# Performance work log

Hardware: AMD Instinct MI355X
Metric: run time of the kernel (lower is better)

Reference implementation:

```python
import jax, jax.numpy as jnp
import numpy as np

B, N, EM = 16, 1024, 768
D_K, D_V, H = 768, 768, 12

def setup_inputs() -> dict:
    key = jax.random.key(0)
    ks = jax.random.split(key, 4)
    s = 0.02
    x = jax.random.normal(ks[0], (B, N, EM), dtype=jnp.float32)
    W_qk = jax.random.normal(ks[1], (EM, 2 * D_K), dtype=jnp.float32) * s
    b_qk = jnp.zeros((2 * D_K,), dtype=jnp.float32)
    W_v = jax.random.normal(ks[2], (EM, D_V), dtype=jnp.float32) * s
    b_v = jnp.zeros((D_V,), dtype=jnp.float32)
    W_proj = jax.random.normal(ks[3], (D_V, EM), dtype=jnp.float32) * s
    b_proj = jnp.zeros((EM,), dtype=jnp.float32)
    return {"x": x, "W_qk": W_qk, "b_qk": b_qk, "W_v": W_v, "b_v": b_v,
            "W_proj": W_proj, "b_proj": b_proj}

def reference(x, W_qk, b_qk, W_v, b_v, W_proj, b_proj):
    b, n, _ = x.shape
    d = D_K // H  # per-head dim
    # qk Linear -> [B,N,2*d_K]; rearrange 'b n (h d qk) -> qk b h n d'
    # i.e. last dim splits as (h, d, 2) with qk fastest-varying.
    qk = (x @ W_qk + b_qk).reshape(b, n, H, d, 2)
    Q = jnp.transpose(qk[..., 0], (0, 2, 1, 3))  # [B,H,N,d]
    K = jnp.transpose(qk[..., 1], (0, 2, 1, 3))  # [B,H,N,d]
    V = (x @ W_v + b_v).reshape(b, n, H, D_V // H).transpose(0, 2, 1, 3)  # [B,H,N,dv]
    scores = jnp.einsum('bhqd,bhkd->bhqk', Q, K) / jnp.sqrt(jnp.float32(d))
    att = jax.nn.softmax(scores, axis=-1)  # dropout p=0 -> identity
    out = jnp.einsum('bhqk,bhkv->bhqv', att, V)  # [B,H,N,dv]
    out = out.transpose(0, 2, 1, 3).reshape(b, n, D_V)
    return out @ W_proj + b_proj
```

## Files before the change

kernel.cpp:

```cpp
#include <hip/hip_runtime.h>
#include <hip/hip_bf16.h>
#include <stdint.h>

typedef unsigned short u16;
typedef __bf16 bf16_t;
typedef bf16_t bf16x8 __attribute__((ext_vector_type(8)));
typedef short s16x4 __attribute__((ext_vector_type(4)));
typedef float f32x4 __attribute__((ext_vector_type(4)));

__device__ __forceinline__ float bf2f(u16 u) {
    union { uint32_t i; float f; } v; v.i = ((uint32_t)u) << 16; return v.f;
}
__device__ __forceinline__ u16 f2bf(float f) {
    union { float f; uint32_t i; } v; v.f = f;
    uint32_t i = v.i;
    uint32_t r = (i + 0x7FFFu + ((i >> 16) & 1u)) >> 16;
    return (u16)r;
}

__device__ __forceinline__ void gload_lds16(const u16* g, u16* l) {
    auto gp = (const __attribute__((address_space(1))) void*)g;
    auto lp = (__attribute__((address_space(3))) void*)(uintptr_t)l;
    __builtin_amdgcn_global_load_lds(gp, lp, 16, 0, 0);
}

__global__ void convert_f32_bf16_kernel(const float* __restrict__ src,
                                        u16* __restrict__ dst, int n4) {
    int i = blockIdx.x * blockDim.x + threadIdx.x;
    if (i < n4) {
        float4 v = ((const float4*)src)[i];
        ushort4 o;
        o.x = f2bf(v.x); o.y = f2bf(v.y); o.z = f2bf(v.z); o.w = f2bf(v.w);
        ((ushort4*)dst)[i] = o;
    }
}

__global__ void transpose_qk_kernel(const float* __restrict__ W, const float* __restrict__ b,
                                    u16* __restrict__ Wt, float* __restrict__ bp) {
    int r = blockIdx.x;
    int qk = (r >= 768) ? 1 : 0;
    int hd = r - qk * 768;
    int c = (hd >> 6) * 128 + (hd & 63) * 2 + qk;
    float s = qk ? 1.0f : 0.125f;
    for (int k = threadIdx.x; k < 768; k += 256)
        Wt[r * 768 + k] = f2bf(s * W[k * 1536 + c]);
    if (threadIdx.x == 0) bp[r] = s * b[c];
}

__global__ void transpose_sq_kernel(const float* __restrict__ W, u16* __restrict__ Wt) {
    int n = blockIdx.x;
    for (int k = threadIdx.x; k < 768; k += 256)
        Wt[n * 768 + k] = f2bf(W[k * 768 + n]);
}

#define BM 128
#define BN 128
#define BK 32
#define LDT 40

template<int MODE>
__global__ __launch_bounds__(256)
void gemm_bt_kernel(const u16* __restrict__ A, const u16* __restrict__ Bt,
                    const float* __restrict__ bias, void* __restrict__ Cout,
                    void* __restrict__ Cout2, int M, int N, int K) {
    __shared__ __attribute__((aligned(16))) u16 As[BM * LDT];
    __shared__ __attribute__((aligned(16))) u16 Bs[BN * LDT];

    const int tid  = threadIdx.x;
    const int lane = tid & 63;
    const int wave = tid >> 6;
    const int l16  = lane & 15;
    const int quad = lane >> 4;
    const int m0 = blockIdx.y * BM;
    const int n0 = blockIdx.x * BN;
    const int wm = (wave & 1) * 64;
    const int wn = (wave >> 1) * 64;

    f32x4 acc[4][4];
#pragma unroll
    for (int i = 0; i < 4; i++)
#pragma unroll
        for (int j = 0; j < 4; j++) acc[i][j] = (f32x4){0.f, 0.f, 0.f, 0.f};

    const int r0  = tid >> 2;
    const int seg = tid & 3;

    for (int k0 = 0; k0 < K; k0 += BK) {
        const u16* Ag = A  + (size_t)(m0 + r0) * K + k0 + seg * 8;
        const u16* Bg = Bt + (size_t)(n0 + r0) * K + k0 + seg * 8;
        int4 a0 = *(const int4*)Ag;
        int4 a1 = *(const int4*)(Ag + (size_t)64 * K);
        int4 b0 = *(const int4*)Bg;
        int4 b1 = *(const int4*)(Bg + (size_t)64 * K);
        *(int4*)&As[r0 * LDT + seg * 8]        = a0;
        *(int4*)&As[(r0 + 64) * LDT + seg * 8] = a1;
        *(int4*)&Bs[r0 * LDT + seg * 8]        = b0;
        *(int4*)&Bs[(r0 + 64) * LDT + seg * 8] = b1;
        __syncthreads();

        bf16x8 af[4], bfr[4];
#pragma unroll
        for (int i = 0; i < 4; i++) {
            af[i]  = *(const bf16x8*)&As[(wm + i * 16 + l16) * LDT + quad * 8];
            bfr[i] = *(const bf16x8*)&Bs[(wn + i * 16 + l16) * LDT + quad * 8];
        }
#pragma unroll
        for (int i = 0; i < 4; i++)
#pragma unroll
            for (int j = 0; j < 4; j++)
                acc[i][j] = __builtin_amdgcn_mfma_f32_16x16x32_bf16(af[i], bfr[j], acc[i][j], 0, 0, 0);
        __syncthreads();
    }

#pragma unroll
    for (int j = 0; j < 4; j++) {
        int cnb = n0 + wn + j * 16;
        int cn  = cnb + l16;
        float bv = bias[cn];
#pragma unroll
        for (int i = 0; i < 4; i++) {
            int cm = m0 + wm + i * 16 + quad * 4;
            if constexpr (MODE == 3) {
                int h  = cnb >> 6;
                int dv = (cnb & 63) + l16;
                int b  = cm >> 10, n = cm & 1023;
                ushort4 o;
                o.x = f2bf(acc[i][j][0] + bv);
                o.y = f2bf(acc[i][j][1] + bv);
                o.z = f2bf(acc[i][j][2] + bv);
                o.w = f2bf(acc[i][j][3] + bv);
                *(ushort4*)&((u16*)Cout)[((size_t)((b * 12 + h) * 64 + dv)) * 1024 + n] = o;
            } else if constexpr (MODE == 2) {
                int qk = cnb >= 768;
                int hd = cnb - qk * 768;
                int h  = hd >> 6;
                int d  = (hd & 63) + l16;
                int b  = cm >> 10, n = cm & 1023;
                u16* dst = (u16*)(qk ? Cout2 : Cout);
#pragma unroll
                for (int r = 0; r < 4; r++)
                    dst[((size_t)((b * 12 + h) * 1024 + n + r)) * 64 + d] =
                        f2bf(acc[i][j][r] + bv);
            } else {
#pragma unroll
                for (int r = 0; r < 4; r++) {
                    float val = acc[i][j][r] + bv;
                    if constexpr (MODE == 1)
                        ((float*)Cout)[(size_t)(cm + r) * N + cn] = val;
                    else
                        ((u16*)Cout)[(size_t)(cm + r) * N + cn] = f2bf(val);
                }
            }
        }
    }
}

__global__ __launch_bounds__(256)
void attention_mfma_kernel(const u16* __restrict__ Qp, const u16* __restrict__ Kp,
                           const u16* __restrict__ Vp, u16* __restrict__ attout) {
    __shared__ __attribute__((aligned(16))) u16 Ks[64 * 64];
    __shared__ __attribute__((aligned(16))) u16 Vs[64 * 64];

    const int tid  = threadIdx.x;
    const int wave = tid >> 6;
    const int lane = tid & 63;
    const int l16  = lane & 15;
    const int quad = lane >> 4;
    const int bh = blockIdx.y;
    const int b  = bh / 12, h = bh % 12;
    const int head = b * 12 + h;
    const int q0 = blockIdx.x * 128 + wave * 32;

    const u16* Qhead = Qp + (size_t)head * 1024 * 64;
    const u16* Khead = Kp + (size_t)head * 1024 * 64;
    const u16* Vhead = Vp + (size_t)head * 64 * 1024;

    bf16x8 qf[2][2];
#pragma unroll
    for (int qb = 0; qb < 2; qb++) {
        const u16* qrow = Qhead + (size_t)(q0 + qb * 16 + l16) * 64;
        qf[qb][0] = *(const bf16x8*)(qrow + quad * 8);
        qf[qb][1] = *(const bf16x8*)(qrow + 32 + quad * 8);
    }

    f32x4 oacc[2][4];
#pragma unroll
    for (int qb = 0; qb < 2; qb++)
#pragma unroll
        for (int db = 0; db < 4; db++) oacc[qb][db] = (f32x4){0.f, 0.f, 0.f, 0.f};
    float l_part[2] = {0.f, 0.f};

    const int srow = tid >> 3;
    const int gseg = (tid & 7) ^ (srow & 7);
    u16* KsW = Ks + wave * 512;
    u16* VsW = Vs + wave * 512;
    const int sw7 = l16 & 7;

    for (int kt = 0; kt < 1024; kt += 64) {
        gload_lds16(Khead + (size_t)(kt + srow) * 64 + gseg * 8,        KsW);
        gload_lds16(Khead + (size_t)(kt + 32 + srow) * 64 + gseg * 8,   KsW + 2048);
        gload_lds16(Vhead + (size_t)srow * 1024 + kt + gseg * 8,        VsW);
        gload_lds16(Vhead + (size_t)(32 + srow) * 1024 + kt + gseg * 8, VsW + 2048);
        __syncthreads();

        s16x4 pf[2][4];
        {
            bf16x8 kf[4][2];
#pragma unroll
            for (int jb = 0; jb < 4; jb++) {
#pragma unroll
                for (int hf = 0; hf < 2; hf++)
                    kf[jb][hf] = *(const bf16x8*)&Ks[(jb * 16 + l16) * 64 +
                                                     (((hf * 4 + quad) ^ sw7) * 8)];
            }
#pragma unroll
            for (int qb = 0; qb < 2; qb++) {
#pragma unroll
                for (int jb = 0; jb < 4; jb++) {
                    f32x4 st = (f32x4){0.f, 0.f, 0.f, 0.f};
                    st = __builtin_amdgcn_mfma_f32_16x16x32_bf16(kf[jb][0], qf[qb][0], st, 0, 0, 0);
                    st = __builtin_amdgcn_mfma_f32_16x16x32_bf16(kf[jb][1], qf[qb][1], st, 0, 0, 0);
                    float e0 = __expf(st[0]), e1 = __expf(st[1]);
                    float e2 = __expf(st[2]), e3 = __expf(st[3]);
                    l_part[qb] += (e0 + e1) + (e2 + e3);
                    union { __hip_bfloat162 h2; uint32_t u; } c0, c1;
                    c0.h2 = __float22bfloat162_rn(make_float2(e0, e1));
                    c1.h2 = __float22bfloat162_rn(make_float2(e2, e3));
                    union { uint32_t u2[2]; s16x4 v; } pk;
                    pk.u2[0] = c0.u; pk.u2[1] = c1.u;
                    pf[qb][jb] = pk.v;
                }
            }
        }

#pragma unroll
        for (int db = 0; db < 4; db++) {
            s16x4 vb[4];
#pragma unroll
            for (int jb = 0; jb < 4; jb++) {
                int g = jb * 2 + (quad >> 1);
                vb[jb] = *(const s16x4*)&Vs[(db * 16 + l16) * 64 +
                                            ((g ^ sw7) * 8) + (quad & 1) * 4];
            }
#pragma unroll
            for (int qb = 0; qb < 2; qb++)
#pragma unroll
                for (int jb = 0; jb < 4; jb++)
                    oacc[qb][db] = __builtin_amdgcn_mfma_f32_16x16x16bf16_1k(
                        pf[qb][jb], vb[jb], oacc[qb][db], 0, 0, 0);
        }
        __syncthreads();
    }

#pragma unroll
    for (int qb = 0; qb < 2; qb++) {
        float l = l_part[qb];
        l += __shfl_xor(l, 16);
        l += __shfl_xor(l, 32);
        float linv[4];
#pragma unroll
        for (int r = 0; r < 4; r++)
            linv[r] = 1.0f / __shfl(l, quad * 4 + r);
        u16* orow = attout + (size_t)(b * 1024 + q0 + qb * 16 + quad * 4) * 768 + h * 64 + l16;
#pragma unroll
        for (int db = 0; db < 4; db++)
#pragma unroll
            for (int r = 0; r < 4; r++)
                orow[(size_t)r * 768 + db * 16] = f2bf(oacc[qb][db][r] * linv[r]);
    }
}

extern "C" void kernel_launch(void* const* d_in, const int* in_sizes, int n_in,
                              void* d_out, int out_size, void* d_ws, size_t ws_size,
                              hipStream_t stream) {
    const float* x      = (const float*)d_in[0];
    const float* W_qk   = (const float*)d_in[1];
    const float* b_qk   = (const float*)d_in[2];
    const float* W_v    = (const float*)d_in[3];
    const float* b_v    = (const float*)d_in[4];
    const float* W_proj = (const float*)d_in[5];
    const float* b_proj = (const float*)d_in[6];
    float* out = (float*)d_out;

    char* ws = (char*)d_ws;
    size_t off = 0;
    auto alloc = [&](size_t bytes) { void* p = ws + off; off += (bytes + 255) & ~255ull; return p; };
    u16*   xb     = (u16*)alloc((size_t)16384 * 768 * 2);
    u16*   Wqkt   = (u16*)alloc((size_t)1536 * 768 * 2);
    float* bqkp   = (float*)alloc(1536 * 4);
    u16*   Wvt    = (u16*)alloc((size_t)768 * 768 * 2);
    u16*   Wprojt = (u16*)alloc((size_t)768 * 768 * 2);
    u16*   Qp     = (u16*)alloc((size_t)16384 * 768 * 2);
    u16*   Kp     = (u16*)alloc((size_t)16384 * 768 * 2);
    u16*   Vp     = (u16*)alloc((size_t)16384 * 768 * 2);
    u16*   attout = (u16*)alloc((size_t)16384 * 768 * 2);

    convert_f32_bf16_kernel<<<12288, 256, 0, stream>>>(x, xb, 3145728);
    transpose_qk_kernel<<<1536, 256, 0, stream>>>(W_qk, b_qk, Wqkt, bqkp);
    transpose_sq_kernel<<<768, 256, 0, stream>>>(W_v, Wvt);
    transpose_sq_kernel<<<768, 256, 0, stream>>>(W_proj, Wprojt);

    gemm_bt_kernel<2><<<dim3(12, 128), 256, 0, stream>>>(xb, Wqkt, bqkp, Qp, Kp, 16384, 1536, 768);
    gemm_bt_kernel<3><<<dim3(6, 128), 256, 0, stream>>>(xb, Wvt, b_v, Vp, nullptr, 16384, 768, 768);
    attention_mfma_kernel<<<dim3(8, 192), 256, 0, stream>>>(Qp, Kp, Vp, attout);
    gemm_bt_kernel<1><<<dim3(6, 128), 256, 0, stream>>>(attout, Wprojt, b_proj, out, nullptr, 16384, 768, 768);
}
```

Measured before the change: 364.7 us.

## Use direct global-to-LDS loads in GEMM, vectorize epilogues, widen attention blocks

The GEMM kernel now stages A and B tiles with global_load_lds instead of register round-trips, using an XOR-swizzled unpadded LDS layout to avoid bank conflicts. For non-V modes it swaps the MFMA operands so each lane holds four consecutive output columns, which allows float4 bias loads and ushort4/float4 vectorized stores. Attention blocks grow to 512 threads covering 256 queries, so each K/V tile loaded into LDS is shared by twice as many waves and each thread issues half as many loads. Risks include lower occupancy from the larger blocks and the unchanged single-buffered GEMM loop still stalling on each barrier.

```diff
diff --git a/kernel.cpp b/kernel.cpp
--- a/kernel.cpp
+++ b/kernel.cpp
@@ -8,9 +8,6 @@
 typedef short s16x4 __attribute__((ext_vector_type(4)));
 typedef float f32x4 __attribute__((ext_vector_type(4)));
 
-__device__ __forceinline__ float bf2f(u16 u) {
-    union { uint32_t i; float f; } v; v.i = ((uint32_t)u) << 16; return v.f;
-}
 __device__ __forceinline__ u16 f2bf(float f) {
     union { float f; uint32_t i; } v; v.f = f;
     uint32_t i = v.i;
@@ -53,26 +50,21 @@
         Wt[n * 768 + k] = f2bf(W[k * 768 + n]);
 }
 
-#define BM 128
-#define BN 128
-#define BK 32
-#define LDT 40
-
 template<int MODE>
 __global__ __launch_bounds__(256)
 void gemm_bt_kernel(const u16* __restrict__ A, const u16* __restrict__ Bt,
                     const float* __restrict__ bias, void* __restrict__ Cout,
                     void* __restrict__ Cout2, int M, int N, int K) {
-    __shared__ __attribute__((aligned(16))) u16 As[BM * LDT];
-    __shared__ __attribute__((aligned(16))) u16 Bs[BN * LDT];
+    __shared__ __attribute__((aligned(16))) u16 As[128 * 32];
+    __shared__ __attribute__((aligned(16))) u16 Bs[128 * 32];
 
     const int tid  = threadIdx.x;
     const int lane = tid & 63;
     const int wave = tid >> 6;
     const int l16  = lane & 15;
     const int quad = lane >> 4;
-    const int m0 = blockIdx.y * BM;
-    const int n0 = blockIdx.x * BN;
+    const int m0 = blockIdx.y * 128;
+    const int n0 = blockIdx.x * 128;
     const int wm = (wave & 1) * 64;
     const int wn = (wave >> 1) * 64;
 
@@ -82,80 +74,99 @@
 #pragma unroll
         for (int j = 0; j < 4; j++) acc[i][j] = (f32x4){0.f, 0.f, 0.f, 0.f};
 
-    const int r0  = tid >> 2;
-    const int seg = tid & 3;
-
-    for (int k0 = 0; k0 < K; k0 += BK) {
-        const u16* Ag = A  + (size_t)(m0 + r0) * K + k0 + seg * 8;
-        const u16* Bg = Bt + (size_t)(n0 + r0) * K + k0 + seg * 8;
-        int4 a0 = *(const int4*)Ag;
-        int4 a1 = *(const int4*)(Ag + (size_t)64 * K);
-        int4 b0 = *(const int4*)Bg;
-        int4 b1 = *(const int4*)(Bg + (size_t)64 * K);
-        *(int4*)&As[r0 * LDT + seg * 8]        = a0;
-        *(int4*)&As[(r0 + 64) * LDT + seg * 8] = a1;
-        *(int4*)&Bs[r0 * LDT + seg * 8]        = b0;
-        *(int4*)&Bs[(r0 + 64) * LDT + seg * 8] = b1;
+    const int rs = lane >> 2;
+    const int sA = (lane & 3) ^ ((lane >> 3) & 3);
+    const u16* Ag0 = A  + (size_t)(m0 + wave * 32 + rs) * K + sA * 8;
+    const u16* Ag1 = Ag0 + (size_t)16 * K;
+    const u16* Bg0 = Bt + (size_t)(n0 + wave * 32 + rs) * K + sA * 8;
+    const u16* Bg1 = Bg0 + (size_t)16 * K;
+    u16* AsW = As + wave * 1024;
+    u16* BsW = Bs + wave * 1024;
+    const int swq = (l16 >> 1) & 3;
+
+    for (int k0 = 0; k0 < K; k0 += 32) {
+        gload_lds16(Ag0 + k0, AsW);
+        gload_lds16(Ag1 + k0, AsW + 512);
+        gload_lds16(Bg0 + k0, BsW);
+        gload_lds16(Bg1 + k0, BsW + 512);
         __syncthreads();
 
         bf16x8 af[4], bfr[4];
 #pragma unroll
         for (int i = 0; i < 4; i++) {
-            af[i]  = *(const bf16x8*)&As[(wm + i * 16 + l16) * LDT + quad * 8];
-            bfr[i] = *(const bf16x8*)&Bs[(wn + i * 16 + l16) * LDT + quad * 8];
+            af[i]  = *(const bf16x8*)&As[(wm + i * 16 + l16) * 32 + ((quad ^ swq) * 8)];
+            bfr[i] = *(const bf16x8*)&Bs[(wn + i * 16 + l16) * 32 + ((quad ^ swq) * 8)];
         }
 #pragma unroll
         for (int i = 0; i < 4; i++)
 #pragma unroll
-            for (int j = 0; j < 4; j++)
-                acc[i][j] = __builtin_amdgcn_mfma_f32_16x16x32_bf16(af[i], bfr[j], acc[i][j], 0, 0, 0);
+            for (int j = 0; j < 4; j++) {
+                if constexpr (MODE == 3)
+                    acc[i][j] = __builtin_amdgcn_mfma_f32_16x16x32_bf16(af[i], bfr[j], acc[i][j], 0, 0, 0);
+                else
+                    acc[i][j] = __builtin_amdgcn_mfma_f32_16x16x32_bf16(bfr[j], af[i], acc[i][j], 0, 0, 0);
+            }
         __syncthreads();
     }
 
-#pragma unroll
-    for (int j = 0; j < 4; j++) {
-        int cnb = n0 + wn + j * 16;
-        int cn  = cnb + l16;
-        float bv = bias[cn];
-#pragma unroll
-        for (int i = 0; i < 4; i++) {
-            int cm = m0 + wm + i * 16 + quad * 4;
-            if constexpr (MODE == 3) {
-                int h  = cnb >> 6;
-                int dv = (cnb & 63) + l16;
-                int b  = cm >> 10, n = cm & 1023;
+    if constexpr (MODE == 3) {
+#pragma unroll
+        for (int j = 0; j < 4; j++) {
+            int cnb = n0 + wn + j * 16;
+            int h   = cnb >> 6;
+            int dv  = (cnb & 63) + l16;
+            float bv = bias[cnb + l16];
+#pragma unroll
+            for (int i = 0; i < 4; i++) {
+                int cm = m0 + wm + i * 16 + quad * 4;
+                int bb = cm >> 10, n = cm & 1023;
                 ushort4 o;
                 o.x = f2bf(acc[i][j][0] + bv);
                 o.y = f2bf(acc[i][j][1] + bv);
                 o.z = f2bf(acc[i][j][2] + bv);
                 o.w = f2bf(acc[i][j][3] + bv);
-                *(ushort4*)&((u16*)Cout)[((size_t)((b * 12 + h) * 64 + dv)) * 1024 + n] = o;
-            } else if constexpr (MODE == 2) {
-                int qk = cnb >= 768;
-                int hd = cnb - qk * 768;
+                *(ushort4*)&((u16*)Cout)[((size_t)((bb * 12 + h) * 64 + dv)) * 1024 + n] = o;
+            }
+        }
+    } else {
+#pragma unroll
+        for (int j = 0; j < 4; j++) {
+            int f0 = n0 + wn + j * 16 + quad * 4;
+            float4 bv = *(const float4*)&bias[f0];
+            if constexpr (MODE == 2) {
+                int qk = f0 >= 768;
+                int hd = f0 - qk * 768;
                 int h  = hd >> 6;
-                int d  = (hd & 63) + l16;
-                int b  = cm >> 10, n = cm & 1023;
+                int d0 = hd & 63;
                 u16* dst = (u16*)(qk ? Cout2 : Cout);
 #pragma unroll
-                for (int r = 0; r < 4; r++)
-                    dst[((size_t)((b * 12 + h) * 1024 + n + r)) * 64 + d] =
-                        f2bf(acc[i][j][r] + bv);
+                for (int i = 0; i < 4; i++) {
+                    int t = m0 + wm + i * 16 + l16;
+                    int bb = t >> 10, n = t & 1023;
+                    ushort4 o;
+                    o.x = f2bf(acc[i][j][0] + bv.x);
+                    o.y = f2bf(acc[i][j][1] + bv.y);
+                    o.z = f2bf(acc[i][j][2] + bv.z);
+                    o.w = f2bf(acc[i][j][3] + bv.w);
+                    *(ushort4*)&dst[((size_t)((bb * 12 + h) * 1024 + n)) * 64 + d0] = o;
+                }
             } else {
 #pragma unroll
-                for (int r = 0; r < 4; r++) {
-                    float val = acc[i][j][r] + bv;
-                    if constexpr (MODE == 1)
-                        ((float*)Cout)[(size_t)(cm + r) * N + cn] = val;
-                    else
-                        ((u16*)Cout)[(size_t)(cm + r) * N + cn] = f2bf(val);
+                for (int i = 0; i < 4; i++) {
+                    int t = m0 + wm + i * 16 + l16;
+                    float4 o;
+                    o.x = acc[i][j][0] + bv.x;
+                    o.y = acc[i][j][1] + bv.y;
+                    o.z = acc[i][j][2] + bv.z;
+                    o.w = acc[i][j][3] + bv.w;
+                    *(float4*)&((float*)Cout)[(size_t)t * N + f0] = o;
                 }
             }
         }
     }
 }
 
-__global__ __launch_bounds__(256)
+__global__ __launch_bounds__(512)
 void attention_mfma_kernel(const u16* __restrict__ Qp, const u16* __restrict__ Kp,
                            const u16* __restrict__ Vp, u16* __restrict__ attout) {
     __shared__ __attribute__((aligned(16))) u16 Ks[64 * 64];
@@ -168,12 +179,11 @@
     const int quad = lane >> 4;
     const int bh = blockIdx.y;
     const int b  = bh / 12, h = bh % 12;
-    const int head = b * 12 + h;
-    const int q0 = blockIdx.x * 128 + wave * 32;
-
-    const u16* Qhead = Qp + (size_t)head * 1024 * 64;
-    const u16* Khead = Kp + (size_t)head * 1024 * 64;
-    const u16* Vhead = Vp + (size_t)head * 64 * 1024;
+    const int q0 = blockIdx.x * 256 + wave * 32;
+
+    const u16* Qhead = Qp + (size_t)bh * 1024 * 64;
+    const u16* Khead = Kp + (size_t)bh * 1024 * 64;
+    const u16* Vhead = Vp + (size_t)bh * 64 * 1024;
 
     bf16x8 qf[2][2];
 #pragma unroll
@@ -197,10 +207,8 @@
     const int sw7 = l16 & 7;
 
     for (int kt = 0; kt < 1024; kt += 64) {
-        gload_lds16(Khead + (size_t)(kt + srow) * 64 + gseg * 8,        KsW);
-        gload_lds16(Khead + (size_t)(kt + 32 + srow) * 64 + gseg * 8,   KsW + 2048);
-        gload_lds16(Vhead + (size_t)srow * 1024 + kt + gseg * 8,        VsW);
-        gload_lds16(Vhead + (size_t)(32 + srow) * 1024 + kt + gseg * 8, VsW + 2048);
+        gload_lds16(Khead + (size_t)(kt + srow) * 64 + gseg * 8, KsW);
+        gload_lds16(Vhead + (size_t)srow * 1024 + kt + gseg * 8, VsW);
         __syncthreads();
 
         s16x4 pf[2][4];
@@ -302,6 +310,6 @@
 
     gemm_bt_kernel<2><<<dim3(12, 128), 256, 0, stream>>>(xb, Wqkt, bqkp, Qp, Kp, 16384, 1536, 768);
     gemm_bt_kernel<3><<<dim3(6, 128), 256, 0, stream>>>(xb, Wvt, b_v, Vp, nullptr, 16384, 768, 768);
-    attention_mfma_kernel<<<dim3(8, 192), 256, 0, stream>>>(Qp, Kp, Vp, attout);
+    attention_mfma_kernel<<<dim3(4, 192), 512, 0, stream>>>(Qp, Kp, Vp, attout);
     gemm_bt_kernel<1><<<dim3(6, 128), 256, 0, stream>>>(attout, Wprojt, b_proj, out, nullptr, 16384, 768, 768);
 }
```

New measurement: 355.0 us. 2.7% less time.
